# Kernel optimization log

Measured on AMD Instinct MI355X. Metric: run time of the kernel, lower is better.

The kernel has to match this reference:

```python
import jax, jax.numpy as jnp
import numpy as np

IN_DIM, OUT_DIM = 1024, 1024
GRID_SIZE, K = 8, 3
TOKENS = 8192


def b_splines(x, grid, k):
    # x: [B, in_dim], grid: [in_dim, grid_size + 2k + 1]
    x = x[..., None]  # [B, in_dim, 1]
    # order-0 indicator bases: [B, in_dim, grid_size + 2k]
    bases = ((x >= grid[:, :-1]) & (x < grid[:, 1:])).astype(x.dtype)
    # Cox-de Boor recursion up to order k -> [B, in_dim, grid_size + k]
    for kk in range(1, k + 1):
        left = (x - grid[:, : -(kk + 1)]) / (grid[:, kk:-1] - grid[:, : -(kk + 1)])
        right = (grid[:, kk + 1:] - x) / (grid[:, kk + 1:] - grid[:, 1:-kk])
        bases = left * bases[..., :-1] + right * bases[..., 1:]
    return bases


def setup_inputs() -> dict:
    key = jax.random.key(0)
    k1, k2, k3 = jax.random.split(key, 3)
    x = jax.random.normal(k1, (TOKENS, IN_DIM), dtype=jnp.float32)
    # grid buffer: arange(-k, grid_size+k+1) * step + grid_range[0], repeated per in_dim
    grid_range = (-1.0, 1.0)
    step = (grid_range[1] - grid_range[0]) / GRID_SIZE
    grid_row = np.arange(-K, GRID_SIZE + K + 1, dtype=np.float32) * step + grid_range[0]
    grid = jnp.asarray(np.tile(grid_row, (IN_DIM, 1)))  # [in_dim, 15]
    coeff = jax.random.normal(k2, (OUT_DIM, IN_DIM, GRID_SIZE + K), dtype=jnp.float32) * 0.1
    scale_base = 1.0 / np.sqrt(IN_DIM) + jax.random.normal(k3, (OUT_DIM, IN_DIM), dtype=jnp.float32) * 0.1
    scale_spline = jnp.ones((1,), dtype=jnp.float32)
    return {"x": x, "grid": grid, "coeff": coeff, "scale_base": scale_base,
            "scale_spline": scale_spline}


def reference(x, grid, coeff, scale_base, scale_spline):
    splines = b_splines(x, grid, K)                      # [B, in, G+K]
    y_b = jnp.matmul(jax.nn.silu(x), scale_base.T)       # [B, out]
    w = coeff * scale_spline                             # scalar broadcast [out, in, G+K]
    y_spline = jnp.einsum('big,oig->bo', splines, w)     # [B, out]
    return y_b + y_spline
```

## Files before the change

kernel.cpp:

```cpp
#include <hip/hip_runtime.h>
#include <hip/hip_bf16.h>
#include <stdint.h>

typedef __attribute__((ext_vector_type(8))) short short8;
typedef __attribute__((ext_vector_type(16))) float floatx16;
typedef unsigned short u16;

#define IN_DIM  1024
#define OUT_DIM 1024
#define NG      11
#define GK      12
#define KDIM    (IN_DIM * GK)
#define TOKENS  8192

#define GBK     64
#define G2R     9
#define G2OPS   36
#define ABUF    (256 * 72)

#define FBK     48
#define FROW    56
#define FBUF    (256 * FROW)
#define FOPS    4

__device__ __forceinline__ u16 f2bf(float f) {
  uint32_t u = __float_as_uint(f);
  uint32_t r = (u + 0x7fffu + ((u >> 16) & 1u)) >> 16;
  return (u16)r;
}

__device__ __forceinline__ void expand_regs(float x, float g0, float inv_h,
                                            uint64_t& V0, uint64_t& V1, uint64_t& V2)
{
  float t  = (x - g0) * inv_h;
  float fc = floorf(t);
  int   c  = (int)fc;
  float u  = t - fc;
  float u2 = u * u;
  float w1 = 1.0f - u;
  float b0 = (w1 * w1 * w1) * (1.0f / 6.0f);
  float b1 = (0.5f * u - 1.0f) * u2 + (2.0f / 3.0f);
  float b2 = ((-0.5f * u + 0.5f) * u + 0.5f) * u + (1.0f / 6.0f);
  float b3 = (u2 * u) * (1.0f / 6.0f);
  float sil = x / (1.0f + __expf(-x));

  uint64_t P = (uint64_t)f2bf(b0) | ((uint64_t)f2bf(b1) << 16)
             | ((uint64_t)f2bf(b2) << 32) | ((uint64_t)f2bf(b3) << 48);
  int  k  = c - 3;
  bool cv = (c >= 0) && (c <= 13);
  int  kneg = (k < 0) ? -k : 0;
  uint64_t Pc = cv ? (P >> (16 * kneg)) : 0ull;
  uint32_t sh = (uint32_t)(16 * ((k < 0) ? 0 : k));

  V0 = (sh < 64)  ? (Pc << (sh & 63)) : 0ull;
  V1 = (sh == 0)  ? 0ull :
       (sh < 64)  ? (Pc >> ((64 - sh) & 63)) :
       (sh < 128) ? (Pc << ((sh - 64) & 63)) : 0ull;
  V2 = (sh <= 64) ? 0ull :
       (sh < 128) ? (Pc >> ((128 - sh) & 63)) :
                    (Pc << ((sh - 128) & 63));
  V2 = (V2 & 0x0000FFFFFFFFFFFFull) | ((uint64_t)f2bf(sil) << 48);
}

__device__ __forceinline__ void async16(const u16* g, u16* l) {
  __builtin_amdgcn_global_load_lds(
      (const __attribute__((address_space(1))) uint32_t*)g,
      (__attribute__((address_space(3))) uint32_t*)l,
      16, 0, 0);
}

__global__ __launch_bounds__(256) void prep_kernel(
    const float* __restrict__ coeff, const float* __restrict__ sb,
    const float* __restrict__ ss_p, u16* __restrict__ Wt,
    const float* __restrict__ X, const float* __restrict__ grid,
    u16* __restrict__ Aexp)
{
  __shared__ __align__(16) char smem_c[24576];
  const int tid = threadIdx.x;

  if (blockIdx.x < 4096) {
    float* cf = (float*)smem_c;
    u16*   st = (u16*)(smem_c + 11264);
    const int b   = blockIdx.x;
    const int o   = b >> 2;
    const int i0  = (b & 3) * 256;
    const float* cbase = coeff + (size_t)o * (IN_DIM * NG) + (size_t)i0 * NG;
#pragma unroll
    for (int p = 0; p < NG; ++p) cf[p * 256 + tid] = cbase[p * 256 + tid];
    const float ss  = ss_p[0];
    const float sbv = sb[(size_t)o * IN_DIM + i0 + tid];
    __syncthreads();
    const float* cp = cf + tid * NG;
    u16 h[GK];
#pragma unroll
    for (int g = 0; g < NG; ++g) h[g] = f2bf(cp[g] * ss);
    h[NG] = f2bf(sbv);
    uint64_t V0 = (uint64_t)h[0] | ((uint64_t)h[1] << 16) | ((uint64_t)h[2] << 32) | ((uint64_t)h[3] << 48);
    uint64_t V1 = (uint64_t)h[4] | ((uint64_t)h[5] << 16) | ((uint64_t)h[6] << 32) | ((uint64_t)h[7] << 48);
    uint64_t V2 = (uint64_t)h[8] | ((uint64_t)h[9] << 16) | ((uint64_t)h[10] << 32) | ((uint64_t)h[11] << 48);
    uint64_t* sp = (uint64_t*)(st + tid * GK);
    sp[0] = V0; sp[1] = V1; sp[2] = V2;
    __syncthreads();
    const uint4* src = (const uint4*)st;
    uint4* dst = (uint4*)(Wt + (size_t)b * (256 * GK));
    dst[tid] = src[tid];
    if (tid < 128) dst[256 + tid] = src[256 + tid];
  } else {
    uint4* st4 = (uint4*)smem_c;
    const float g0    = grid[0];
    const float inv_h = 1.0f / (grid[1] - grid[0]);
    const int bb = blockIdx.x - 4096;
    for (int rr = 0; rr < 4; ++rr) {
      const int row = bb * 4 + rr;
      float4 xv = *(const float4*)(X + (size_t)row * IN_DIM + tid * 4);
      uint64_t ev[12];
      expand_regs(xv.x, g0, inv_h, ev[0], ev[1], ev[2]);
      expand_regs(xv.y, g0, inv_h, ev[3], ev[4], ev[5]);
      expand_regs(xv.z, g0, inv_h, ev[6], ev[7], ev[8]);
      expand_regs(xv.w, g0, inv_h, ev[9], ev[10], ev[11]);
      if (rr) __syncthreads();
#pragma unroll
      for (int j = 0; j < 6; ++j) {
        uint4 w;
        w.x = (uint32_t)ev[2*j];     w.y = (uint32_t)(ev[2*j] >> 32);
        w.z = (uint32_t)ev[2*j+1];   w.w = (uint32_t)(ev[2*j+1] >> 32);
        st4[tid * 6 + j] = w;
      }
      __syncthreads();
      uint4* dst = (uint4*)(Aexp + (size_t)row * KDIM);
#pragma unroll
      for (int j = 0; j < 6; ++j) dst[j * 256 + tid] = st4[j * 256 + tid];
    }
  }
}

__global__ __launch_bounds__(512, 2) void gemm_pre_kernel(
    const u16* __restrict__ A, const u16* __restrict__ Wt,
    float* __restrict__ out, float* __restrict__ part, int k_iters)
{
  __shared__ __align__(16) u16 S[4 * ABUF];

  const int tid  = threadIdx.x;
  const int lane = tid & 63;
  const int wave = tid >> 6;
  const int s    = (blockIdx.x >> 2) & 1;
  const int bn   = blockIdx.x & 3;
  const int bm   = blockIdx.x >> 3;
  const int wm   = (wave >> 2) * 128;
  const int wn   = (wave & 3) * 64;
  const int l31  = lane & 31;
  const int g8   = lane >> 5;

  floatx16 acc[4][2];
#pragma unroll
  for (int a = 0; a < 4; ++a)
#pragma unroll
    for (int b = 0; b < 2; ++b)
#pragma unroll
      for (int rr = 0; rr < 16; ++rr) acc[a][b][rr] = 0.f;

  const size_t k0 = (size_t)s * k_iters * GBK;
  const u16* src[9]; int dof[9];
#pragma unroll
  for (int j = 0; j < 9; ++j) {
    int q    = wave + 8 * j;
    bool isA = (q < 36);
    int oq   = isA ? q : q - 36;
    int gidx  = oq * 64 + lane;
    int row   = gidx / 9;
    int chunk = gidx - row * 9;
    int c8    = (chunk == 8) ? 0 : chunk;
    src[j] = (isA ? A + (size_t)(bm * 256 + row) * KDIM
                  : Wt + (size_t)(bn * 256 + row) * KDIM) + k0 + c8 * 8;
    dof[j] = (isA ? 0 : 2 * ABUF) + oq * 512;
  }

  const int NT = k_iters;

#pragma unroll
  for (int j = 0; j < 9; ++j) async16(src[j], S + dof[j]);
  asm volatile("s_waitcnt vmcnt(0)" ::: "memory");
  __builtin_amdgcn_s_barrier();
  __builtin_amdgcn_sched_barrier(0);
#pragma unroll
  for (int j = 0; j < 9; ++j) async16(src[j] + GBK, S + ABUF + dof[j]);

  for (int t = 0; t < NT; ++t) {
    const u16* Ab = S + (t & 1) * ABUF;
    const u16* Bb = S + 2 * ABUF + (t & 1) * ABUF;

    __builtin_amdgcn_s_setprio(1);
#pragma unroll
    for (int ks = 0; ks < 4; ++ks) {
      short8 bf0 = *(const short8*)&Bb[(wn +      l31) * 72 + (2 * ks + g8) * 8];
      short8 bf1 = *(const short8*)&Bb[(wn + 32 + l31) * 72 + (2 * ks + g8) * 8];
#pragma unroll
      for (int m = 0; m < 4; ++m) {
        short8 af = *(const short8*)&Ab[(wm + m * 32 + l31) * 72 + (2 * ks + g8) * 8];
        acc[m][0] = __builtin_amdgcn_mfma_f32_32x32x16_bf16(af, bf0, acc[m][0], 0, 0, 0);
        acc[m][1] = __builtin_amdgcn_mfma_f32_32x32x16_bf16(af, bf1, acc[m][1], 0, 0, 0);
      }
    }
    __builtin_amdgcn_s_setprio(0);

    __builtin_amdgcn_s_barrier();
    __builtin_amdgcn_sched_barrier(0);
    if (t + 2 < NT) {
      u16* D = S + (t & 1) * ABUF;
      const size_t ko = (size_t)(t + 2) * GBK;
#pragma unroll
      for (int j = 0; j < 9; ++j) async16(src[j] + ko, D + dof[j]);
      asm volatile("s_waitcnt vmcnt(9)" ::: "memory");
    } else {
      asm volatile("s_waitcnt vmcnt(0)" ::: "memory");
    }
    __builtin_amdgcn_s_barrier();
    __builtin_amdgcn_sched_barrier(0);
  }

  float* op = (s == 0) ? out : part;
#pragma unroll
  for (int m = 0; m < 4; ++m)
#pragma unroll
    for (int n = 0; n < 2; ++n) {
      const int row0 = bm * 256 + wm + m * 32 + 4 * g8;
      const int col  = bn * 256 + wn + n * 32 + l31;
#pragma unroll
      for (int reg = 0; reg < 16; ++reg) {
        int row = row0 + (reg & 3) + 8 * (reg >> 2);
        op[(size_t)row * OUT_DIM + col] = acc[m][n][reg];
      }
    }
}

__global__ __launch_bounds__(256) void reduce_kernel(
    float* __restrict__ out, const float* __restrict__ part)
{
  size_t i = (size_t)blockIdx.x * 256 + threadIdx.x;
  float4* o = (float4*)out;
  const float4* p = (const float4*)part;
  float4 a = o[i], b = p[i];
  a.x += b.x; a.y += b.y; a.z += b.z; a.w += b.w;
  o[i] = a;
}

__device__ __forceinline__ void expand2(float2 xv, float g0, float inv_h, uint64_t e[6]) {
  expand_regs(xv.x, g0, inv_h, e[0], e[1], e[2]);
  expand_regs(xv.y, g0, inv_h, e[3], e[4], e[5]);
}
__device__ __forceinline__ void write_ev(u16* abase, int awoff, const uint64_t e[6]) {
  uint4* w = (uint4*)(abase + awoff);
  uint4 w0, w1, w2;
  w0.x = (uint32_t)e[0]; w0.y = (uint32_t)(e[0] >> 32);
  w0.z = (uint32_t)e[1]; w0.w = (uint32_t)(e[1] >> 32);
  w1.x = (uint32_t)e[2]; w1.y = (uint32_t)(e[2] >> 32);
  w1.z = (uint32_t)e[3]; w1.w = (uint32_t)(e[3] >> 32);
  w2.x = (uint32_t)e[4]; w2.y = (uint32_t)(e[4] >> 32);
  w2.z = (uint32_t)e[5]; w2.w = (uint32_t)(e[5] >> 32);
  w[0] = w0; w[1] = w1; w[2] = w2;
}

__global__ __launch_bounds__(256) void pack_wt_kernel(
    const float* __restrict__ coeff, const float* __restrict__ sb,
    const float* __restrict__ ss_p, u16* __restrict__ Wt)
{
  __shared__ float cf[256 * NG];
  __shared__ __align__(16) u16 st[256 * GK];
  const int tid = threadIdx.x;
  const int b   = blockIdx.x;
  const int o   = b >> 2;
  const int i0  = (b & 3) * 256;
  const float* cbase = coeff + (size_t)o * (IN_DIM * NG) + (size_t)i0 * NG;
#pragma unroll
  for (int p = 0; p < NG; ++p) cf[p * 256 + tid] = cbase[p * 256 + tid];
  const float ss  = ss_p[0];
  const float sbv = sb[(size_t)o * IN_DIM + i0 + tid];
  __syncthreads();
  const float* cp = cf + tid * NG;
  u16 h[GK];
#pragma unroll
  for (int g = 0; g < NG; ++g) h[g] = f2bf(cp[g] * ss);
  h[NG] = f2bf(sbv);
  uint64_t V0 = (uint64_t)h[0] | ((uint64_t)h[1] << 16) | ((uint64_t)h[2] << 32) | ((uint64_t)h[3] << 48);
  uint64_t V1 = (uint64_t)h[4] | ((uint64_t)h[5] << 16) | ((uint64_t)h[6] << 32) | ((uint64_t)h[7] << 48);
  uint64_t V2 = (uint64_t)h[8] | ((uint64_t)h[9] << 16) | ((uint64_t)h[10] << 32) | ((uint64_t)h[11] << 48);
  uint64_t* sp = (uint64_t*)(st + tid * GK);
  sp[0] = V0; sp[1] = V1; sp[2] = V2;
  __syncthreads();
  const uint4* src = (const uint4*)st;
  uint4* dst = (uint4*)(Wt + (size_t)b * (256 * GK));
  dst[tid] = src[tid];
  if (tid < 128) dst[256 + tid] = src[256 + tid];
}

__global__ __launch_bounds__(512, 2) void gemm_fused2_kernel(
    const float* __restrict__ X, const float* __restrict__ grid,
    const u16* __restrict__ Wt, float* __restrict__ out, float* __restrict__ part,
    int k_iters)
{
  __shared__ __align__(16) u16 S[4 * FBUF];

  const int tid  = threadIdx.x;
  const int lane = tid & 63;
  const int wave = tid >> 6;
  const int s    = blockIdx.x >> 7;
  const int r    = blockIdx.x & 127;
  const int bm   = r & 31;
  const int bn   = r >> 5;
  const int wm   = (wave >> 2) * 128;
  const int wn   = (wave & 3) * 64;
  const int l31  = lane & 31;
  const int g8   = lane >> 5;

  const float g0    = grid[0];
  const float inv_h = 1.0f / (grid[1] - grid[0]);

  floatx16 acc[4][2];
#pragma unroll
  for (int a = 0; a < 4; ++a)
#pragma unroll
    for (int b = 0; b < 2; ++b)
#pragma unroll
      for (int rr = 0; rr < 16; ++rr) acc[a][b][rr] = 0.f;

  const int kb = s * k_iters * FBK;
  const u16* bsrc[FOPS]; int bdof[FOPS];
#pragma unroll
  for (int j = 0; j < FOPS; ++j) {
    int o  = wave + 8 * j;
    int oc = (o < 28) ? o : 27;
    int gidx = oc * 64 + lane;
    int row  = gidx / 7;
    int sl   = gidx - row * 7;
    int c6   = (sl == 6) ? 0 : sl;
    bsrc[j] = Wt + (size_t)(bn * 256 + row) * KDIM + kb + c6 * 8;
    bdof[j] = oc * 512;
  }

  const int arow  = tid >> 1;
  const int cp    = (tid & 1) * 2;
  const float* xp = X + (size_t)(bm * 256 + arow) * IN_DIM + s * (k_iters * 4) + cp;
  const int awoff = arow * FROW + cp * 12;

  const int NT = k_iters;

  float2 x0    = *(const float2*)(xp + 0);
  float2 x1    = *(const float2*)(xp + 4);
  float2 x_use = *(const float2*)(xp + 8);
  float2 x_mid = *(const float2*)(xp + 12);
  float2 x_new = x_use;

#pragma unroll
  for (int j = 0; j < FOPS; ++j) async16(bsrc[j],       S + 2 * FBUF + bdof[j]);
#pragma unroll
  for (int j = 0; j < FOPS; ++j) async16(bsrc[j] + FBK, S + 3 * FBUF + bdof[j]);
  {
    uint64_t e[6];
    expand2(x0, g0, inv_h, e); write_ev(S, awoff, e);
    expand2(x1, g0, inv_h, e); write_ev(S + FBUF, awoff, e);
  }
  asm volatile("s_waitcnt vmcnt(0) lgkmcnt(0)" ::: "memory");
  __builtin_amdgcn_s_barrier();
  __builtin_amdgcn_sched_barrier(0);

  for (int t = 0; t < NT; ++t) {
    const int p = t & 1;
    const u16* Ab = S + p * FBUF;
    const u16* Bb = S + 2 * FBUF + p * FBUF;

    uint64_t e[6];
    const bool dostage = (t + 2 < NT);
    if (dostage) expand2(x_use, g0, inv_h, e);

    __builtin_amdgcn_s_setprio(1);
#pragma unroll
    for (int ks = 0; ks < 3; ++ks) {
      const int cc = (2 * ks + g8) * 8;
      short8 bf0 = *(const short8*)&Bb[(wn +      l31) * FROW + cc];
      short8 bf1 = *(const short8*)&Bb[(wn + 32 + l31) * FROW + cc];
#pragma unroll
      for (int m = 0; m < 4; ++m) {
        short8 af = *(const short8*)&Ab[(wm + m * 32 + l31) * FROW + cc];
        acc[m][0] = __builtin_amdgcn_mfma_f32_32x32x16_bf16(af, bf0, acc[m][0], 0, 0, 0);
        acc[m][1] = __builtin_amdgcn_mfma_f32_32x32x16_bf16(af, bf1, acc[m][1], 0, 0, 0);
      }
    }
    __builtin_amdgcn_s_setprio(0);

    __builtin_amdgcn_s_barrier();
    __builtin_amdgcn_sched_barrier(0);

    if (dostage) {
      const int ko = (t + 2) * FBK;
      u16* Bd = S + 2 * FBUF + p * FBUF;
#pragma unroll
      for (int j = 0; j < FOPS; ++j) async16(bsrc[j] + ko, Bd + bdof[j]);
      write_ev(S + p * FBUF, awoff, e);
      if (t + 4 < NT) {
        x_new = *(const float2*)(xp + (size_t)(t + 4) * 4);
        asm volatile("s_waitcnt vmcnt(5) lgkmcnt(0)" ::: "memory");
      } else {
        asm volatile("s_waitcnt vmcnt(4) lgkmcnt(0)" ::: "memory");
      }
    } else {
      asm volatile("s_waitcnt vmcnt(0) lgkmcnt(0)" ::: "memory");
    }
    __builtin_amdgcn_s_barrier();
    __builtin_amdgcn_sched_barrier(0);

    x_use = x_mid; x_mid = x_new;
  }

  float* op = (s == 0) ? out : part;
#pragma unroll
  for (int m = 0; m < 4; ++m)
#pragma unroll
    for (int n = 0; n < 2; ++n) {
      const int row0 = bm * 256 + wm + m * 32 + 4 * g8;
      const int col  = bn * 256 + wn + n * 32 + l31;
#pragma unroll
      for (int reg = 0; reg < 16; ++reg) {
        int row = row0 + (reg & 3) + 8 * (reg >> 2);
        op[(size_t)row * OUT_DIM + col] = acc[m][n][reg];
      }
    }
}

extern "C" void kernel_launch(void* const* d_in, const int* in_sizes, int n_in,
                              void* d_out, int out_size, void* d_ws, size_t ws_size,
                              hipStream_t stream) {
  const float* x     = (const float*)d_in[0];
  const float* grid  = (const float*)d_in[1];
  const float* coeff = (const float*)d_in[2];
  const float* sb    = (const float*)d_in[3];
  const float* ss    = (const float*)d_in[4];
  float* out = (float*)d_out;

  u16* Wt = (u16*)d_ws;
  const size_t wt_bytes   = (size_t)OUT_DIM * KDIM * 2;
  const size_t aexp_bytes = (size_t)TOKENS * KDIM * 2;
  const size_t part_bytes = (size_t)TOKENS * OUT_DIM * 4;

  if (ws_size >= wt_bytes + aexp_bytes + part_bytes) {
    u16*   Aexp = (u16*)((char*)d_ws + wt_bytes);
    float* part = (float*)((char*)d_ws + wt_bytes + aexp_bytes);
    prep_kernel<<<4096 + TOKENS / 4, 256, 0, stream>>>(coeff, sb, ss, Wt, x, grid, Aexp);
    gemm_pre_kernel<<<256, 512, 0, stream>>>(Aexp, Wt, out, part, 96);
    reduce_kernel<<<(TOKENS * OUT_DIM / 4) / 256, 256, 0, stream>>>(out, part);
  } else if (ws_size >= wt_bytes + part_bytes) {
    float* part = (float*)((char*)d_ws + wt_bytes);
    pack_wt_kernel<<<(OUT_DIM * IN_DIM) / 256, 256, 0, stream>>>(coeff, sb, ss, Wt);
    gemm_fused2_kernel<<<128 * 2, 512, 0, stream>>>(x, grid, Wt, out, part, 128);
    reduce_kernel<<<(TOKENS * OUT_DIM / 4) / 256, 256, 0, stream>>>(out, part);
  } else {
    pack_wt_kernel<<<(OUT_DIM * IN_DIM) / 256, 256, 0, stream>>>(coeff, sb, ss, Wt);
    gemm_fused2_kernel<<<128, 512, 0, stream>>>(x, grid, Wt, out, nullptr, 256);
  }
}
```

Baseline: 382.8 us.

## Double-buffer expansion rows in prep kernel and remap GEMM block indices

```diff
diff --git a/kernel.cpp b/kernel.cpp
--- a/kernel.cpp
+++ b/kernel.cpp
@@ -75,7 +75,7 @@
     const float* __restrict__ X, const float* __restrict__ grid,
     u16* __restrict__ Aexp)
 {
-  __shared__ __align__(16) char smem_c[24576];
+  __shared__ __align__(16) char smem_c[49152];
   const int tid = threadIdx.x;
 
   if (blockIdx.x < 4096) {
@@ -106,30 +106,54 @@
     dst[tid] = src[tid];
     if (tid < 128) dst[256 + tid] = src[256 + tid];
   } else {
-    uint4* st4 = (uint4*)smem_c;
+    uint4 (*st4)[1536] = (uint4 (*)[1536])smem_c;
     const float g0    = grid[0];
     const float inv_h = 1.0f / (grid[1] - grid[0]);
-    const int bb = blockIdx.x - 4096;
-    for (int rr = 0; rr < 4; ++rr) {
-      const int row = bb * 4 + rr;
-      float4 xv = *(const float4*)(X + (size_t)row * IN_DIM + tid * 4);
-      uint64_t ev[12];
+    const int bb   = blockIdx.x - 4096;
+    const int row0 = bb * 8;
+
+    uint64_t ev[12];
+    {
+      float4 xv = *(const float4*)(X + (size_t)row0 * IN_DIM + tid * 4);
       expand_regs(xv.x, g0, inv_h, ev[0], ev[1], ev[2]);
       expand_regs(xv.y, g0, inv_h, ev[3], ev[4], ev[5]);
       expand_regs(xv.z, g0, inv_h, ev[6], ev[7], ev[8]);
       expand_regs(xv.w, g0, inv_h, ev[9], ev[10], ev[11]);
-      if (rr) __syncthreads();
 #pragma unroll
       for (int j = 0; j < 6; ++j) {
         uint4 w;
         w.x = (uint32_t)ev[2*j];     w.y = (uint32_t)(ev[2*j] >> 32);
         w.z = (uint32_t)ev[2*j+1];   w.w = (uint32_t)(ev[2*j+1] >> 32);
-        st4[tid * 6 + j] = w;
+        st4[0][tid * 6 + j] = w;
+      }
+    }
+    __syncthreads();
+
+    for (int rr = 0; rr < 8; ++rr) {
+      const int p = rr & 1;
+      uint4 v[6];
+#pragma unroll
+      for (int j = 0; j < 6; ++j) v[j] = st4[p][j * 256 + tid];
+      if (rr + 1 < 8) {
+        float4 xv = *(const float4*)(X + (size_t)(row0 + rr + 1) * IN_DIM + tid * 4);
+        expand_regs(xv.x, g0, inv_h, ev[0], ev[1], ev[2]);
+        expand_regs(xv.y, g0, inv_h, ev[3], ev[4], ev[5]);
+        expand_regs(xv.z, g0, inv_h, ev[6], ev[7], ev[8]);
+        expand_regs(xv.w, g0, inv_h, ev[9], ev[10], ev[11]);
+      }
+      uint4* dst = (uint4*)(Aexp + (size_t)(row0 + rr) * KDIM);
+#pragma unroll
+      for (int j = 0; j < 6; ++j) dst[j * 256 + tid] = v[j];
+      if (rr + 1 < 8) {
+#pragma unroll
+        for (int j = 0; j < 6; ++j) {
+          uint4 w;
+          w.x = (uint32_t)ev[2*j];     w.y = (uint32_t)(ev[2*j] >> 32);
+          w.z = (uint32_t)ev[2*j+1];   w.w = (uint32_t)(ev[2*j+1] >> 32);
+          st4[p ^ 1][tid * 6 + j] = w;
+        }
       }
       __syncthreads();
-      uint4* dst = (uint4*)(Aexp + (size_t)row * KDIM);
-#pragma unroll
-      for (int j = 0; j < 6; ++j) dst[j * 256 + tid] = st4[j * 256 + tid];
     }
   }
 }
@@ -143,9 +167,10 @@
   const int tid  = threadIdx.x;
   const int lane = tid & 63;
   const int wave = tid >> 6;
-  const int s    = (blockIdx.x >> 2) & 1;
-  const int bn   = blockIdx.x & 3;
-  const int bm   = blockIdx.x >> 3;
+  const int s    = blockIdx.x >> 7;
+  const int r    = blockIdx.x & 127;
+  const int bm   = r & 31;
+  const int bn   = r >> 5;
   const int wm   = (wave >> 2) * 128;
   const int wn   = (wave & 3) * 64;
   const int l31  = lane & 31;
@@ -444,8 +469,8 @@
   if (ws_size >= wt_bytes + aexp_bytes + part_bytes) {
     u16*   Aexp = (u16*)((char*)d_ws + wt_bytes);
     float* part = (float*)((char*)d_ws + wt_bytes + aexp_bytes);
-    prep_kernel<<<4096 + TOKENS / 4, 256, 0, stream>>>(coeff, sb, ss, Wt, x, grid, Aexp);
-    gemm_pre_kernel<<<256, 512, 0, stream>>>(Aexp, Wt, out, part, 96);
+    prep_kernel<<<4096 + TOKENS / 8, 256, 0, stream>>>(coeff, sb, ss, Wt, x, grid, Aexp);
+    gemm_pre_kernel<<<128 * 2, 512, 0, stream>>>(Aexp, Wt, out, part, 96);
     reduce_kernel<<<(TOKENS * OUT_DIM / 4) / 256, 256, 0, stream>>>(out, part);
   } else if (ws_size >= wt_bytes + part_bytes) {
     float* part = (float*)((char*)d_ws + wt_bytes);
```

Measured after the change: 368.1 us. -3.9%, faster.
